# Kernel optimization log

Hardware: AMD Instinct MI355X
Metric: run time of the kernel (lower is better)

## Reference

```python
import jax, jax.numpy as jnp
import numpy as np

HOP_NUM = 3
N_NODES = 40000
N_EDGES = 640000
IN_DIM = 128
N_ALPHAS = HOP_NUM * (HOP_NUM + 1) // 2  # triangular layerRegular params


def setup_inputs() -> dict:
    key = jax.random.key(0)
    k_h, k_d, k_a, k_s, k_t = jax.random.split(key, 5)
    h = jax.random.normal(k_h, (N_NODES, IN_DIM), dtype=jnp.float32)
    d = jax.random.uniform(k_d, (N_NODES,), dtype=jnp.float32)  # degree normalization per node
    alphas = jax.random.uniform(k_a, (N_ALPHAS,), dtype=jnp.float32)
    src = jax.random.randint(k_s, (N_EDGES,), 0, N_NODES, dtype=jnp.int32)
    dst = jax.random.randint(k_t, (N_EDGES,), 0, N_NODES, dtype=jnp.int32)
    return {"h": h, "d": d, "alphas": alphas, "src": src, "dst": dst}


def reference(h, d, alphas, src, dst):
    n = h.shape[0]
    # edge_applying: e = 1 * d[dst] * d[src]  (symmetric-normalized edge weight)
    e = d[dst] * d[src]                      # [E]
    outs = [h]
    k = 0
    for i in range(HOP_NUM):
        feat = h
        for q in range(i + 1):
            # update_all(u_mul_e('h','e'), sum): agg[v] = sum_{(u,v)} feat[u] * e
            msg = feat[src] * e[:, None]     # [E, D]
            agg = jax.ops.segment_sum(msg, dst, num_segments=n)  # [N, D]
            a = alphas[k]; k += 1
            feat = agg * a + (1.0 - a) * feat
            # feature_drop with p=0.0 (eval) is identity
        outs.append(feat)
    return jnp.concatenate(outs, axis=1)       # [N, (HOP_NUM+1)*D]
```

## Files before the change

### kernel.cpp

```cpp
#include <hip/hip_runtime.h>


#define NN  40000
#define NE  640000
#define CAP 64

__device__ inline unsigned short f2h(float f) {
    _Float16 h = (_Float16)f;
    return *(unsigned short*)&h;
}
__device__ inline float h2f(unsigned short u) {
    _Float16 h = *(_Float16*)&u;
    return (float)h;
}
__device__ inline unsigned short f2bf(float f) {
    unsigned int x = __float_as_uint(f);
    x += 0x7fffu + ((x >> 16) & 1u);
    return (unsigned short)(x >> 16);
}
__device__ inline unsigned int pack_bf2(float x, float y) {
    return ((unsigned int)f2bf(y) << 16) | (unsigned int)f2bf(x);
}
__device__ inline float bflo(unsigned int u) { return __uint_as_float(u << 16); }
__device__ inline float bfhi(unsigned int u) { return __uint_as_float(u & 0xffff0000u); }

__global__ __launch_bounds__(256) void build_buckets_k(
    const int* __restrict__ src, const int* __restrict__ dst,
    const float* __restrict__ deg,
    int* __restrict__ counts, unsigned int* __restrict__ buck) {
    int e = blockIdx.x * 256 + threadIdx.x;
    if (e >= NE) return;
    int s = src[e];
    int v = dst[e];
    int slot = atomicAdd(&counts[v], 1);
    if (slot < CAP) {
        float w = deg[s] * deg[v];
        buck[v * CAP + slot] = ((unsigned int)f2h(w) << 16) | (unsigned int)s;
    }
}

__global__ __launch_bounds__(256) void cvt_h_k(
    const float* __restrict__ h, unsigned int* __restrict__ hb) {
    int i = blockIdx.x * 256 + threadIdx.x;
    if (i >= NN * 64) return;
    float2 f = *(const float2*)(h + (size_t)i * 2);
    hb[i] = pack_bf2(f.x, f.y);
}

__device__ inline float2 gather_node(
    const unsigned int* __restrict__ feat,
    const int* __restrict__ counts, const unsigned int* __restrict__ buck,
    int v, int lane) {
    int cnt = counts[v];
    if (cnt > CAP) cnt = CAP;
    unsigned int myw = buck[(size_t)v * CAP + lane];
    if (lane >= cnt) myw = 0u;
    float ax = 0.f, ay = 0.f, bx = 0.f, by = 0.f;
    for (int j = 0; j < cnt; j += 4) {
        unsigned int u0 = __shfl(myw, j + 0);
        unsigned int u1 = __shfl(myw, j + 1);
        unsigned int u2 = __shfl(myw, j + 2);
        unsigned int u3 = __shfl(myw, j + 3);
        unsigned int f0 = feat[(size_t)(u0 & 0xffffu) * 64 + lane];
        unsigned int f1 = feat[(size_t)(u1 & 0xffffu) * 64 + lane];
        unsigned int f2 = feat[(size_t)(u2 & 0xffffu) * 64 + lane];
        unsigned int f3 = feat[(size_t)(u3 & 0xffffu) * 64 + lane];
        float w0 = h2f((unsigned short)(u0 >> 16));
        float w1 = h2f((unsigned short)(u1 >> 16));
        float w2 = h2f((unsigned short)(u2 >> 16));
        float w3 = h2f((unsigned short)(u3 >> 16));
        ax = fmaf(w0, bflo(f0), ax); ay = fmaf(w0, bfhi(f0), ay);
        bx = fmaf(w1, bflo(f1), bx); by = fmaf(w1, bfhi(f1), by);
        ax = fmaf(w2, bflo(f2), ax); ay = fmaf(w2, bfhi(f2), ay);
        bx = fmaf(w3, bflo(f3), bx); by = fmaf(w3, bfhi(f3), by);
    }
    return make_float2(ax + bx, ay + by);
}

__global__ __launch_bounds__(256) void agg_k(
    const unsigned int* __restrict__ feat,
    const int* __restrict__ counts, const unsigned int* __restrict__ buck,
    unsigned int* __restrict__ outf) {
    int gid  = blockIdx.x * 256 + threadIdx.x;
    int v    = gid >> 6;
    int lane = gid & 63;
    if (v >= NN) return;
    float2 acc = gather_node(feat, counts, buck, v, lane);
    outf[(size_t)v * 64 + lane] = pack_bf2(acc.x, acc.y);
}

__global__ __launch_bounds__(256) void agg3_fused_k(
    const unsigned int* __restrict__ p2b,
    const float* __restrict__ h,
    const unsigned int* __restrict__ p1b,
    const int* __restrict__ counts, const unsigned int* __restrict__ buck,
    const float* __restrict__ alphas, float* __restrict__ out) {
    int gid  = blockIdx.x * 256 + threadIdx.x;
    int v    = gid >> 6;
    int lane = gid & 63;
    if (v >= NN) return;
    float2 p3 = gather_node(p2b, counts, buck, v, lane);

    float a0 = alphas[0], a1 = alphas[1], a2 = alphas[2];
    float a3 = alphas[3], a4 = alphas[4], a5 = alphas[5];
    float c1p = a0, c1h = 1.f - a0;
    float c2pp = a2 * a1;
    float c2p  = a2 * (1.f - a1) + (1.f - a2) * a1;
    float c2h  = (1.f - a2) * (1.f - a1);
    float s2pp = a4 * a3;
    float s2p  = a4 * (1.f - a3) + (1.f - a4) * a3;
    float s2h  = (1.f - a4) * (1.f - a3);
    float c3ppp = a5 * s2pp;
    float c3pp  = a5 * s2p + (1.f - a5) * s2pp;
    float c3p   = a5 * s2h + (1.f - a5) * s2p;
    float c3h   = (1.f - a5) * s2h;

    int i2 = lane * 2;
    float2 hf = *(const float2*)(h + (size_t)v * 128 + i2);
    unsigned int u1 = p1b[(size_t)v * 64 + lane];
    unsigned int u2 = p2b[(size_t)v * 64 + lane];
    float q1x = bflo(u1), q1y = bfhi(u1);
    float q2x = bflo(u2), q2y = bfhi(u2);

    float2 r1, r2, r3;
    r1.x = c1p * q1x + c1h * hf.x;
    r1.y = c1p * q1y + c1h * hf.y;
    r2.x = c2pp * q2x + c2p * q1x + c2h * hf.x;
    r2.y = c2pp * q2y + c2p * q1y + c2h * hf.y;
    r3.x = c3ppp * p3.x + c3pp * q2x + c3p * q1x + c3h * hf.x;
    r3.y = c3ppp * p3.y + c3pp * q2y + c3p * q1y + c3h * hf.y;

    float* o = out + (size_t)v * 512;
    *(float2*)(o + i2)       = hf;
    *(float2*)(o + 128 + i2) = r1;
    *(float2*)(o + 256 + i2) = r2;
    *(float2*)(o + 384 + i2) = r3;
}

extern "C" void kernel_launch(void* const* d_in, const int* in_sizes, int n_in,
                              void* d_out, int out_size, void* d_ws, size_t ws_size,
                              hipStream_t stream) {
    const float* h      = (const float*)d_in[0];
    const float* deg    = (const float*)d_in[1];
    const float* alphas = (const float*)d_in[2];
    const int*   src    = (const int*)d_in[3];
    const int*   dst    = (const int*)d_in[4];
    float* out = (float*)d_out;

    char* ws = (char*)d_ws;
    int*          counts = (int*)(ws + 0);
    unsigned int* buck   = (unsigned int*)(ws + 160000);
    unsigned int* hb     = (unsigned int*)(ws + 10400000);
    unsigned int* p1b    = (unsigned int*)(ws + 20640000);
    unsigned int* p2b    = (unsigned int*)(ws + 30880000);

    hipMemsetAsync(counts, 0, NN * sizeof(int), stream);
    build_buckets_k<<<NE / 256, 256, 0, stream>>>(src, dst, deg, counts, buck);
    cvt_h_k<<<(NN * 64 + 255) / 256, 256, 0, stream>>>(h, hb);

    agg_k<<<NN / 4, 256, 0, stream>>>(hb,  counts, buck, p1b);
    agg_k<<<NN / 4, 256, 0, stream>>>(p1b, counts, buck, p2b);
    agg3_fused_k<<<NN / 4, 256, 0, stream>>>(p2b, h, p1b, counts, buck,
                                             alphas, out);
}
```

Before: 215.9 us.

## Fuse all stages into one cooperative persistent kernel with grid syncs

Replaces the memset plus five separate launches with a single cooperative kernel of 1024 blocks that uses grid-wide syncs between bucket building, h conversion, and the three aggregation hops. The h copy into the output is moved into the conversion stage. The gather loop is unrolled to 8 neighbours with four accumulator pairs for more memory-level parallelism. This is meant to cut launch overhead and inter-kernel gaps, at the cost of grid-sync latency and fixed-grid occupancy limits. It falls back to the multi-kernel path if the cooperative launch fails.

Result: slower. 700.6 us (+224.4%).

```diff
diff --git a/kernel.cpp b/kernel.cpp
--- a/kernel.cpp
+++ b/kernel.cpp
@@ -1,9 +1,14 @@
 #include <hip/hip_runtime.h>
-
-
-#define NN  40000
-#define NE  640000
-#define CAP 64
+#include <hip/hip_cooperative_groups.h>
+
+namespace cg = cooperative_groups;
+
+
+#define NN   40000
+#define NE   640000
+#define CAP  64
+#define GRID 1024
+#define BLK  256
 
 __device__ inline unsigned short f2h(float f) {
     _Float16 h = (_Float16)f;
@@ -23,29 +28,6 @@
 }
 __device__ inline float bflo(unsigned int u) { return __uint_as_float(u << 16); }
 __device__ inline float bfhi(unsigned int u) { return __uint_as_float(u & 0xffff0000u); }
-
-__global__ __launch_bounds__(256) void build_buckets_k(
-    const int* __restrict__ src, const int* __restrict__ dst,
-    const float* __restrict__ deg,
-    int* __restrict__ counts, unsigned int* __restrict__ buck) {
-    int e = blockIdx.x * 256 + threadIdx.x;
-    if (e >= NE) return;
-    int s = src[e];
-    int v = dst[e];
-    int slot = atomicAdd(&counts[v], 1);
-    if (slot < CAP) {
-        float w = deg[s] * deg[v];
-        buck[v * CAP + slot] = ((unsigned int)f2h(w) << 16) | (unsigned int)s;
-    }
-}
-
-__global__ __launch_bounds__(256) void cvt_h_k(
-    const float* __restrict__ h, unsigned int* __restrict__ hb) {
-    int i = blockIdx.x * 256 + threadIdx.x;
-    if (i >= NN * 64) return;
-    float2 f = *(const float2*)(h + (size_t)i * 2);
-    hb[i] = pack_bf2(f.x, f.y);
-}
 
 __device__ inline float2 gather_node(
     const unsigned int* __restrict__ feat,
@@ -56,50 +38,85 @@
     unsigned int myw = buck[(size_t)v * CAP + lane];
     if (lane >= cnt) myw = 0u;
     float ax = 0.f, ay = 0.f, bx = 0.f, by = 0.f;
-    for (int j = 0; j < cnt; j += 4) {
-        unsigned int u0 = __shfl(myw, j + 0);
-        unsigned int u1 = __shfl(myw, j + 1);
-        unsigned int u2 = __shfl(myw, j + 2);
-        unsigned int u3 = __shfl(myw, j + 3);
+    float cx = 0.f, cy = 0.f, dx = 0.f, dy = 0.f;
+    for (int j = 0; j < cnt; j += 8) {
+        unsigned int u0 = __shfl(myw, j + 0), u1 = __shfl(myw, j + 1);
+        unsigned int u2 = __shfl(myw, j + 2), u3 = __shfl(myw, j + 3);
+        unsigned int u4 = __shfl(myw, j + 4), u5 = __shfl(myw, j + 5);
+        unsigned int u6 = __shfl(myw, j + 6), u7 = __shfl(myw, j + 7);
         unsigned int f0 = feat[(size_t)(u0 & 0xffffu) * 64 + lane];
         unsigned int f1 = feat[(size_t)(u1 & 0xffffu) * 64 + lane];
         unsigned int f2 = feat[(size_t)(u2 & 0xffffu) * 64 + lane];
         unsigned int f3 = feat[(size_t)(u3 & 0xffffu) * 64 + lane];
+        unsigned int f4 = feat[(size_t)(u4 & 0xffffu) * 64 + lane];
+        unsigned int f5 = feat[(size_t)(u5 & 0xffffu) * 64 + lane];
+        unsigned int f6 = feat[(size_t)(u6 & 0xffffu) * 64 + lane];
+        unsigned int f7 = feat[(size_t)(u7 & 0xffffu) * 64 + lane];
         float w0 = h2f((unsigned short)(u0 >> 16));
         float w1 = h2f((unsigned short)(u1 >> 16));
         float w2 = h2f((unsigned short)(u2 >> 16));
         float w3 = h2f((unsigned short)(u3 >> 16));
+        float w4 = h2f((unsigned short)(u4 >> 16));
+        float w5 = h2f((unsigned short)(u5 >> 16));
+        float w6 = h2f((unsigned short)(u6 >> 16));
+        float w7 = h2f((unsigned short)(u7 >> 16));
         ax = fmaf(w0, bflo(f0), ax); ay = fmaf(w0, bfhi(f0), ay);
         bx = fmaf(w1, bflo(f1), bx); by = fmaf(w1, bfhi(f1), by);
-        ax = fmaf(w2, bflo(f2), ax); ay = fmaf(w2, bfhi(f2), ay);
-        bx = fmaf(w3, bflo(f3), bx); by = fmaf(w3, bfhi(f3), by);
-    }
-    return make_float2(ax + bx, ay + by);
-}
-
-__global__ __launch_bounds__(256) void agg_k(
-    const unsigned int* __restrict__ feat,
-    const int* __restrict__ counts, const unsigned int* __restrict__ buck,
-    unsigned int* __restrict__ outf) {
-    int gid  = blockIdx.x * 256 + threadIdx.x;
-    int v    = gid >> 6;
-    int lane = gid & 63;
-    if (v >= NN) return;
-    float2 acc = gather_node(feat, counts, buck, v, lane);
-    outf[(size_t)v * 64 + lane] = pack_bf2(acc.x, acc.y);
-}
-
-__global__ __launch_bounds__(256) void agg3_fused_k(
-    const unsigned int* __restrict__ p2b,
-    const float* __restrict__ h,
-    const unsigned int* __restrict__ p1b,
-    const int* __restrict__ counts, const unsigned int* __restrict__ buck,
-    const float* __restrict__ alphas, float* __restrict__ out) {
-    int gid  = blockIdx.x * 256 + threadIdx.x;
-    int v    = gid >> 6;
-    int lane = gid & 63;
-    if (v >= NN) return;
-    float2 p3 = gather_node(p2b, counts, buck, v, lane);
+        cx = fmaf(w2, bflo(f2), cx); cy = fmaf(w2, bfhi(f2), cy);
+        dx = fmaf(w3, bflo(f3), dx); dy = fmaf(w3, bfhi(f3), dy);
+        ax = fmaf(w4, bflo(f4), ax); ay = fmaf(w4, bfhi(f4), ay);
+        bx = fmaf(w5, bflo(f5), bx); by = fmaf(w5, bfhi(f5), by);
+        cx = fmaf(w6, bflo(f6), cx); cy = fmaf(w6, bfhi(f6), cy);
+        dx = fmaf(w7, bflo(f7), dx); dy = fmaf(w7, bfhi(f7), dy);
+    }
+    return make_float2((ax + bx) + (cx + dx), (ay + by) + (cy + dy));
+}
+
+__global__ __launch_bounds__(BLK) void fused_k(
+    const float* __restrict__ h, const float* __restrict__ deg,
+    const float* __restrict__ alphas,
+    const int* __restrict__ src, const int* __restrict__ dst,
+    float* __restrict__ out,
+    int* __restrict__ counts, unsigned int* __restrict__ buck,
+    unsigned int* __restrict__ hb, unsigned int* __restrict__ p1b,
+    unsigned int* __restrict__ p2b) {
+    cg::grid_group grid = cg::this_grid();
+    const int tid  = blockIdx.x * BLK + threadIdx.x;
+    const int nthr = GRID * BLK;
+    const int lane = threadIdx.x & 63;
+    const int wid  = blockIdx.x * (BLK / 64) + (threadIdx.x >> 6);
+    const int nw   = GRID * (BLK / 64);
+
+    if (tid < NN) counts[tid] = 0;
+    for (int i = tid; i < NN * 64; i += nthr) {
+        float2 f = *(const float2*)(h + (size_t)i * 2);
+        hb[i] = pack_bf2(f.x, f.y);
+        int v = i >> 6, w = i & 63;
+        *(float2*)(out + (size_t)v * 512 + w * 2) = f;
+    }
+    grid.sync();
+
+    for (int e = tid; e < NE; e += nthr) {
+        int s = src[e];
+        int v = dst[e];
+        int slot = atomicAdd(&counts[v], 1);
+        if (slot < CAP)
+            buck[v * CAP + slot] =
+                ((unsigned int)f2h(deg[s] * deg[v]) << 16) | (unsigned int)s;
+    }
+    grid.sync();
+
+    for (int v = wid; v < NN; v += nw) {
+        float2 a = gather_node(hb, counts, buck, v, lane);
+        p1b[(size_t)v * 64 + lane] = pack_bf2(a.x, a.y);
+    }
+    grid.sync();
+
+    for (int v = wid; v < NN; v += nw) {
+        float2 a = gather_node(p1b, counts, buck, v, lane);
+        p2b[(size_t)v * 64 + lane] = pack_bf2(a.x, a.y);
+    }
+    grid.sync();
 
     float a0 = alphas[0], a1 = alphas[1], a2 = alphas[2];
     float a3 = alphas[3], a4 = alphas[4], a5 = alphas[5];
@@ -115,13 +132,94 @@
     float c3p   = a5 * s2h + (1.f - a5) * s2p;
     float c3h   = (1.f - a5) * s2h;
 
+    for (int v = wid; v < NN; v += nw) {
+        float2 p3 = gather_node(p2b, counts, buck, v, lane);
+        int i2 = lane * 2;
+        float2 hf = *(const float2*)(h + (size_t)v * 128 + i2);
+        unsigned int u1 = p1b[(size_t)v * 64 + lane];
+        unsigned int u2 = p2b[(size_t)v * 64 + lane];
+        float q1x = bflo(u1), q1y = bfhi(u1);
+        float q2x = bflo(u2), q2y = bfhi(u2);
+        float2 r1, r2, r3;
+        r1.x = c1p * q1x + c1h * hf.x;
+        r1.y = c1p * q1y + c1h * hf.y;
+        r2.x = c2pp * q2x + c2p * q1x + c2h * hf.x;
+        r2.y = c2pp * q2y + c2p * q1y + c2h * hf.y;
+        r3.x = c3ppp * p3.x + c3pp * q2x + c3p * q1x + c3h * hf.x;
+        r3.y = c3ppp * p3.y + c3pp * q2y + c3p * q1y + c3h * hf.y;
+        float* o = out + (size_t)v * 512;
+        *(float2*)(o + 128 + i2) = r1;
+        *(float2*)(o + 256 + i2) = r2;
+        *(float2*)(o + 384 + i2) = r3;
+    }
+}
+
+__global__ __launch_bounds__(256) void build_buckets_k(
+    const int* __restrict__ src, const int* __restrict__ dst,
+    const float* __restrict__ deg,
+    int* __restrict__ counts, unsigned int* __restrict__ buck) {
+    int e = blockIdx.x * 256 + threadIdx.x;
+    if (e >= NE) return;
+    int s = src[e];
+    int v = dst[e];
+    int slot = atomicAdd(&counts[v], 1);
+    if (slot < CAP)
+        buck[v * CAP + slot] =
+            ((unsigned int)f2h(deg[s] * deg[v]) << 16) | (unsigned int)s;
+}
+
+__global__ __launch_bounds__(256) void cvt_h_k(
+    const float* __restrict__ h, unsigned int* __restrict__ hb,
+    float* __restrict__ out) {
+    int i = blockIdx.x * 256 + threadIdx.x;
+    if (i >= NN * 64) return;
+    float2 f = *(const float2*)(h + (size_t)i * 2);
+    hb[i] = pack_bf2(f.x, f.y);
+    int v = i >> 6, w = i & 63;
+    *(float2*)(out + (size_t)v * 512 + w * 2) = f;
+}
+
+__global__ __launch_bounds__(256) void agg_k(
+    const unsigned int* __restrict__ feat,
+    const int* __restrict__ counts, const unsigned int* __restrict__ buck,
+    unsigned int* __restrict__ outf) {
+    int gid  = blockIdx.x * 256 + threadIdx.x;
+    int v    = gid >> 6;
+    int lane = gid & 63;
+    if (v >= NN) return;
+    float2 acc = gather_node(feat, counts, buck, v, lane);
+    outf[(size_t)v * 64 + lane] = pack_bf2(acc.x, acc.y);
+}
+
+__global__ __launch_bounds__(256) void agg3_fused_k(
+    const unsigned int* __restrict__ p2b, const float* __restrict__ h,
+    const unsigned int* __restrict__ p1b,
+    const int* __restrict__ counts, const unsigned int* __restrict__ buck,
+    const float* __restrict__ alphas, float* __restrict__ out) {
+    int gid  = blockIdx.x * 256 + threadIdx.x;
+    int v    = gid >> 6;
+    int lane = gid & 63;
+    if (v >= NN) return;
+    float2 p3 = gather_node(p2b, counts, buck, v, lane);
+    float a0 = alphas[0], a1 = alphas[1], a2 = alphas[2];
+    float a3 = alphas[3], a4 = alphas[4], a5 = alphas[5];
+    float c1p = a0, c1h = 1.f - a0;
+    float c2pp = a2 * a1;
+    float c2p  = a2 * (1.f - a1) + (1.f - a2) * a1;
+    float c2h  = (1.f - a2) * (1.f - a1);
+    float s2pp = a4 * a3;
+    float s2p  = a4 * (1.f - a3) + (1.f - a4) * a3;
+    float s2h  = (1.f - a4) * (1.f - a3);
+    float c3ppp = a5 * s2pp;
+    float c3pp  = a5 * s2p + (1.f - a5) * s2pp;
+    float c3p   = a5 * s2h + (1.f - a5) * s2p;
+    float c3h   = (1.f - a5) * s2h;
     int i2 = lane * 2;
     float2 hf = *(const float2*)(h + (size_t)v * 128 + i2);
     unsigned int u1 = p1b[(size_t)v * 64 + lane];
     unsigned int u2 = p2b[(size_t)v * 64 + lane];
     float q1x = bflo(u1), q1y = bfhi(u1);
     float q2x = bflo(u2), q2y = bfhi(u2);
-
     float2 r1, r2, r3;
     r1.x = c1p * q1x + c1h * hf.x;
     r1.y = c1p * q1y + c1h * hf.y;
@@ -129,9 +227,7 @@
     r2.y = c2pp * q2y + c2p * q1y + c2h * hf.y;
     r3.x = c3ppp * p3.x + c3pp * q2x + c3p * q1x + c3h * hf.x;
     r3.y = c3ppp * p3.y + c3pp * q2y + c3p * q1y + c3h * hf.y;
-
     float* o = out + (size_t)v * 512;
-    *(float2*)(o + i2)       = hf;
     *(float2*)(o + 128 + i2) = r1;
     *(float2*)(o + 256 + i2) = r2;
     *(float2*)(o + 384 + i2) = r3;
@@ -154,12 +250,19 @@
     unsigned int* p1b    = (unsigned int*)(ws + 20640000);
     unsigned int* p2b    = (unsigned int*)(ws + 30880000);
 
-    hipMemsetAsync(counts, 0, NN * sizeof(int), stream);
-    build_buckets_k<<<NE / 256, 256, 0, stream>>>(src, dst, deg, counts, buck);
-    cvt_h_k<<<(NN * 64 + 255) / 256, 256, 0, stream>>>(h, hb);
-
-    agg_k<<<NN / 4, 256, 0, stream>>>(hb,  counts, buck, p1b);
-    agg_k<<<NN / 4, 256, 0, stream>>>(p1b, counts, buck, p2b);
-    agg3_fused_k<<<NN / 4, 256, 0, stream>>>(p2b, h, p1b, counts, buck,
-                                             alphas, out);
-}
+    void* args[] = {(void*)&h,   (void*)&deg, (void*)&alphas, (void*)&src,
+                    (void*)&dst, (void*)&out, (void*)&counts, (void*)&buck,
+                    (void*)&hb,  (void*)&p1b, (void*)&p2b};
+    hipError_t err = hipLaunchCooperativeKernel((const void*)fused_k,
+                                                dim3(GRID), dim3(BLK),
+                                                args, 0, stream);
+    if (err != hipSuccess) {
+        hipMemsetAsync(counts, 0, NN * sizeof(int), stream);
+        build_buckets_k<<<NE / 256, 256, 0, stream>>>(src, dst, deg, counts, buck);
+        cvt_h_k<<<(NN * 64 + 255) / 256, 256, 0, stream>>>(h, hb, out);
+        agg_k<<<NN / 4, 256, 0, stream>>>(hb,  counts, buck, p1b);
+        agg_k<<<NN / 4, 256, 0, stream>>>(p1b, counts, buck, p2b);
+        agg3_fused_k<<<NN / 4, 256, 0, stream>>>(p2b, h, p1b, counts, buck,
+                                                 alphas, out);
+    }
+}
```

## Fuse memset with bf16 convert, unroll gather to 8, spread output writes

Applied to the files above, without the earlier changes.

Replaces the memset and the conversion kernel with one init kernel that zeroes the counts, converts h to bf16 and writes the h slice of the output. The gather loop is unrolled to 8 neighbours with four independent accumulator pairs to keep more loads in flight. The hop-1 and hop-2 output columns are now written in the second aggregation kernel, which leaves only hop 3 for the last kernel. This cuts one launch and spreads the output stores across kernels, at the cost of more registers in the gather.

After: 217.8 us. Within noise of the previous version (+0.8%).

```diff
diff --git a/kernel.cpp b/kernel.cpp
--- a/kernel.cpp
+++ b/kernel.cpp
@@ -24,6 +24,18 @@
 __device__ inline float bflo(unsigned int u) { return __uint_as_float(u << 16); }
 __device__ inline float bfhi(unsigned int u) { return __uint_as_float(u & 0xffff0000u); }
 
+__global__ __launch_bounds__(256) void init_k(
+    const float* __restrict__ h, unsigned int* __restrict__ hb,
+    int* __restrict__ counts, float* __restrict__ out) {
+    int i = blockIdx.x * 256 + threadIdx.x;
+    if (i < NN) counts[i] = 0;
+    if (i >= NN * 64) return;
+    float2 f = *(const float2*)(h + (size_t)i * 2);
+    hb[i] = pack_bf2(f.x, f.y);
+    int v = i >> 6, w = i & 63;
+    *(float2*)(out + (size_t)v * 512 + w * 2) = f;
+}
+
 __global__ __launch_bounds__(256) void build_buckets_k(
     const int* __restrict__ src, const int* __restrict__ dst,
     const float* __restrict__ deg,
@@ -33,18 +45,9 @@
     int s = src[e];
     int v = dst[e];
     int slot = atomicAdd(&counts[v], 1);
-    if (slot < CAP) {
-        float w = deg[s] * deg[v];
-        buck[v * CAP + slot] = ((unsigned int)f2h(w) << 16) | (unsigned int)s;
-    }
-}
-
-__global__ __launch_bounds__(256) void cvt_h_k(
-    const float* __restrict__ h, unsigned int* __restrict__ hb) {
-    int i = blockIdx.x * 256 + threadIdx.x;
-    if (i >= NN * 64) return;
-    float2 f = *(const float2*)(h + (size_t)i * 2);
-    hb[i] = pack_bf2(f.x, f.y);
+    if (slot < CAP)
+        buck[v * CAP + slot] =
+            ((unsigned int)f2h(deg[s] * deg[v]) << 16) | (unsigned int)s;
 }
 
 __device__ inline float2 gather_node(
@@ -56,42 +59,87 @@
     unsigned int myw = buck[(size_t)v * CAP + lane];
     if (lane >= cnt) myw = 0u;
     float ax = 0.f, ay = 0.f, bx = 0.f, by = 0.f;
-    for (int j = 0; j < cnt; j += 4) {
-        unsigned int u0 = __shfl(myw, j + 0);
-        unsigned int u1 = __shfl(myw, j + 1);
-        unsigned int u2 = __shfl(myw, j + 2);
-        unsigned int u3 = __shfl(myw, j + 3);
+    float cx = 0.f, cy = 0.f, dx = 0.f, dy = 0.f;
+    for (int j = 0; j < cnt; j += 8) {
+        unsigned int u0 = __shfl(myw, j + 0), u1 = __shfl(myw, j + 1);
+        unsigned int u2 = __shfl(myw, j + 2), u3 = __shfl(myw, j + 3);
+        unsigned int u4 = __shfl(myw, j + 4), u5 = __shfl(myw, j + 5);
+        unsigned int u6 = __shfl(myw, j + 6), u7 = __shfl(myw, j + 7);
         unsigned int f0 = feat[(size_t)(u0 & 0xffffu) * 64 + lane];
         unsigned int f1 = feat[(size_t)(u1 & 0xffffu) * 64 + lane];
         unsigned int f2 = feat[(size_t)(u2 & 0xffffu) * 64 + lane];
         unsigned int f3 = feat[(size_t)(u3 & 0xffffu) * 64 + lane];
+        unsigned int f4 = feat[(size_t)(u4 & 0xffffu) * 64 + lane];
+        unsigned int f5 = feat[(size_t)(u5 & 0xffffu) * 64 + lane];
+        unsigned int f6 = feat[(size_t)(u6 & 0xffffu) * 64 + lane];
+        unsigned int f7 = feat[(size_t)(u7 & 0xffffu) * 64 + lane];
         float w0 = h2f((unsigned short)(u0 >> 16));
         float w1 = h2f((unsigned short)(u1 >> 16));
         float w2 = h2f((unsigned short)(u2 >> 16));
         float w3 = h2f((unsigned short)(u3 >> 16));
+        float w4 = h2f((unsigned short)(u4 >> 16));
+        float w5 = h2f((unsigned short)(u5 >> 16));
+        float w6 = h2f((unsigned short)(u6 >> 16));
+        float w7 = h2f((unsigned short)(u7 >> 16));
         ax = fmaf(w0, bflo(f0), ax); ay = fmaf(w0, bfhi(f0), ay);
         bx = fmaf(w1, bflo(f1), bx); by = fmaf(w1, bfhi(f1), by);
-        ax = fmaf(w2, bflo(f2), ax); ay = fmaf(w2, bfhi(f2), ay);
-        bx = fmaf(w3, bflo(f3), bx); by = fmaf(w3, bfhi(f3), by);
+        cx = fmaf(w2, bflo(f2), cx); cy = fmaf(w2, bfhi(f2), cy);
+        dx = fmaf(w3, bflo(f3), dx); dy = fmaf(w3, bfhi(f3), dy);
+        ax = fmaf(w4, bflo(f4), ax); ay = fmaf(w4, bfhi(f4), ay);
+        bx = fmaf(w5, bflo(f5), bx); by = fmaf(w5, bfhi(f5), by);
+        cx = fmaf(w6, bflo(f6), cx); cy = fmaf(w6, bfhi(f6), cy);
+        dx = fmaf(w7, bflo(f7), dx); dy = fmaf(w7, bfhi(f7), dy);
     }
-    return make_float2(ax + bx, ay + by);
+    return make_float2((ax + bx) + (cx + dx), (ay + by) + (cy + dy));
 }
 
-__global__ __launch_bounds__(256) void agg_k(
-    const unsigned int* __restrict__ feat,
+__global__ __launch_bounds__(256) void agg1_k(
+    const unsigned int* __restrict__ hb,
     const int* __restrict__ counts, const unsigned int* __restrict__ buck,
-    unsigned int* __restrict__ outf) {
+    unsigned int* __restrict__ p1b) {
     int gid  = blockIdx.x * 256 + threadIdx.x;
     int v    = gid >> 6;
     int lane = gid & 63;
     if (v >= NN) return;
-    float2 acc = gather_node(feat, counts, buck, v, lane);
-    outf[(size_t)v * 64 + lane] = pack_bf2(acc.x, acc.y);
+    float2 a = gather_node(hb, counts, buck, v, lane);
+    p1b[(size_t)v * 64 + lane] = pack_bf2(a.x, a.y);
 }
 
-__global__ __launch_bounds__(256) void agg3_fused_k(
-    const unsigned int* __restrict__ p2b,
-    const float* __restrict__ h,
+__global__ __launch_bounds__(256) void agg2_k(
+    const unsigned int* __restrict__ p1b, const float* __restrict__ h,
+    const int* __restrict__ counts, const unsigned int* __restrict__ buck,
+    const float* __restrict__ alphas,
+    unsigned int* __restrict__ p2b, float* __restrict__ out) {
+    int gid  = blockIdx.x * 256 + threadIdx.x;
+    int v    = gid >> 6;
+    int lane = gid & 63;
+    if (v >= NN) return;
+    float2 p2 = gather_node(p1b, counts, buck, v, lane);
+    p2b[(size_t)v * 64 + lane] = pack_bf2(p2.x, p2.y);
+
+    float a0 = alphas[0], a1 = alphas[1], a2 = alphas[2];
+    float c1p = a0, c1h = 1.f - a0;
+    float c2pp = a2 * a1;
+    float c2p  = a2 * (1.f - a1) + (1.f - a2) * a1;
+    float c2h  = (1.f - a2) * (1.f - a1);
+
+    int i2 = lane * 2;
+    float2 hf = *(const float2*)(h + (size_t)v * 128 + i2);
+    unsigned int u1 = p1b[(size_t)v * 64 + lane];
+    float q1x = bflo(u1), q1y = bfhi(u1);
+
+    float2 r1, r2;
+    r1.x = c1p * q1x + c1h * hf.x;
+    r1.y = c1p * q1y + c1h * hf.y;
+    r2.x = c2pp * p2.x + c2p * q1x + c2h * hf.x;
+    r2.y = c2pp * p2.y + c2p * q1y + c2h * hf.y;
+    float* o = out + (size_t)v * 512;
+    *(float2*)(o + 128 + i2) = r1;
+    *(float2*)(o + 256 + i2) = r2;
+}
+
+__global__ __launch_bounds__(256) void agg3_k(
+    const unsigned int* __restrict__ p2b, const float* __restrict__ h,
     const unsigned int* __restrict__ p1b,
     const int* __restrict__ counts, const unsigned int* __restrict__ buck,
     const float* __restrict__ alphas, float* __restrict__ out) {
@@ -101,12 +149,7 @@
     if (v >= NN) return;
     float2 p3 = gather_node(p2b, counts, buck, v, lane);
 
-    float a0 = alphas[0], a1 = alphas[1], a2 = alphas[2];
     float a3 = alphas[3], a4 = alphas[4], a5 = alphas[5];
-    float c1p = a0, c1h = 1.f - a0;
-    float c2pp = a2 * a1;
-    float c2p  = a2 * (1.f - a1) + (1.f - a2) * a1;
-    float c2h  = (1.f - a2) * (1.f - a1);
     float s2pp = a4 * a3;
     float s2p  = a4 * (1.f - a3) + (1.f - a4) * a3;
     float s2h  = (1.f - a4) * (1.f - a3);
@@ -122,19 +165,10 @@
     float q1x = bflo(u1), q1y = bfhi(u1);
     float q2x = bflo(u2), q2y = bfhi(u2);
 
-    float2 r1, r2, r3;
-    r1.x = c1p * q1x + c1h * hf.x;
-    r1.y = c1p * q1y + c1h * hf.y;
-    r2.x = c2pp * q2x + c2p * q1x + c2h * hf.x;
-    r2.y = c2pp * q2y + c2p * q1y + c2h * hf.y;
+    float2 r3;
     r3.x = c3ppp * p3.x + c3pp * q2x + c3p * q1x + c3h * hf.x;
     r3.y = c3ppp * p3.y + c3pp * q2y + c3p * q1y + c3h * hf.y;
-
-    float* o = out + (size_t)v * 512;
-    *(float2*)(o + i2)       = hf;
-    *(float2*)(o + 128 + i2) = r1;
-    *(float2*)(o + 256 + i2) = r2;
-    *(float2*)(o + 384 + i2) = r3;
+    *(float2*)(out + (size_t)v * 512 + 384 + i2) = r3;
 }
 
 extern "C" void kernel_launch(void* const* d_in, const int* in_sizes, int n_in,
@@ -154,12 +188,9 @@
     unsigned int* p1b    = (unsigned int*)(ws + 20640000);
     unsigned int* p2b    = (unsigned int*)(ws + 30880000);
 
-    hipMemsetAsync(counts, 0, NN * sizeof(int), stream);
+    init_k<<<(NN * 64 + 255) / 256, 256, 0, stream>>>(h, hb, counts, out);
     build_buckets_k<<<NE / 256, 256, 0, stream>>>(src, dst, deg, counts, buck);
-    cvt_h_k<<<(NN * 64 + 255) / 256, 256, 0, stream>>>(h, hb);
-
-    agg_k<<<NN / 4, 256, 0, stream>>>(hb,  counts, buck, p1b);
-    agg_k<<<NN / 4, 256, 0, stream>>>(p1b, counts, buck, p2b);
-    agg3_fused_k<<<NN / 4, 256, 0, stream>>>(p2b, h, p1b, counts, buck,
-                                             alphas, out);
+    agg1_k<<<NN / 4, 256, 0, stream>>>(hb, counts, buck, p1b);
+    agg2_k<<<NN / 4, 256, 0, stream>>>(p1b, h, counts, buck, alphas, p2b, out);
+    agg3_k<<<NN / 4, 256, 0, stream>>>(p2b, h, p1b, counts, buck, alphas, out);
 }
```
